# Performance work log

Hardware: AMD Instinct MI355X
Metric: run time of the kernel (lower is better)

Reference implementation:

```python
import jax, jax.numpy as jnp
import numpy as np

TEMPERATURE = 0.1
WINDOW = 7  # torch loop: k in range(1, min(8, seq_len - i)) -> offsets 1..7


def _normalize(x, axis=-1, eps=1e-12):
    # F.normalize: x / max(||x||, eps)
    n = jnp.linalg.norm(x, axis=axis, keepdims=True)
    return x / jnp.maximum(n, eps)


def setup_inputs() -> dict:
    key = jax.random.key(0)
    k1, k2 = jax.random.split(key, 2)
    states = jax.random.normal(k1, (4, 16, 1024, 256), dtype=jnp.float32)
    patterns = jax.random.normal(k2, (64, 256), dtype=jnp.float32)
    transfer_weights = jnp.zeros((16, 64, 64), dtype=jnp.float32)
    return {"states": states, "patterns": patterns, "transfer_weights": transfer_weights}


def _forward(states, patterns, transfer_weights):
    b, h, s, d = states.shape
    # --- detect_patterns: similarity to normalized pattern library + softmax ---
    sims = jnp.einsum('bhsd,pd->bhsp', states, _normalize(patterns))
    pattern_scores = jax.nn.softmax(sims / TEMPERATURE, axis=-1)  # [b,h,s,p]

    # --- compute_routing_scores: grad of states.sum() wrt states is ones ->
    #     grad_norm = ||ones||_2 over dim = sqrt(d) (constant), softmax over seq ---
    grad_norm = jnp.full((b, h, s), jnp.sqrt(jnp.float32(d)), dtype=states.dtype)
    routing_scores = jax.nn.softmax(grad_norm / TEMPERATURE, axis=-1)  # uniform [b,h,s]

    # --- optimize_routing: windowed min-plus shortest-path DP ---
    # torch keeps distances [b,h,s,s] but every slice along dim 2 is identical
    # (init and updates only index the last axis), so carry a [b,h,s] vector
    # and broadcast at the end. Pad by WINDOW so near-end updates land in pad.
    inf = jnp.float32(np.inf)
    dist0 = jnp.full((b, h, s + WINDOW), inf, dtype=states.dtype).at[..., 0].set(0.0)
    cost_pad = jnp.pad(-routing_scores, ((0, 0), (0, 0), (0, WINDOW)))

    def step(dist, i):
        cur = jax.lax.dynamic_slice_in_dim(dist, i, 1, axis=-1)          # [b,h,1]
        win = jax.lax.dynamic_slice_in_dim(dist, i + 1, WINDOW, axis=-1)  # [b,h,W]
        c = jax.lax.dynamic_slice_in_dim(cost_pad, i + 1, WINDOW, axis=-1)
        new = jnp.minimum(win, cur + c)
        dist = jax.lax.dynamic_update_slice_in_dim(dist, new, i + 1, axis=-1)
        return dist, None

    dist, _ = jax.lax.scan(step, dist0, jnp.arange(s - 1))
    d_final = dist[..., :s]                                  # [b,h,s]
    optimal_routes = jnp.broadcast_to(d_final[:, :, None, :], (b, h, s, s))

    return routing_scores, optimal_routes, transfer_weights, pattern_scores


def reference(states, patterns, transfer_weights):
    return _forward(states, patterns, transfer_weights)
```

## Files before the change

kernel.cpp:

```cpp
#include <hip/hip_runtime.h>
#include <math.h>

constexpr int B = 4, H = 16, S = 1024, D = 256, P = 64;
constexpr long long N_ROWS = (long long)B * H * S;
constexpr long long OFF_RT = 0;
constexpr long long SZ_RT  = N_ROWS;
constexpr long long OFF_OR = OFF_RT + SZ_RT;
constexpr long long SZ_OR  = N_ROWS * (long long)S;
constexpr long long OFF_TW = OFF_OR + SZ_OR;
constexpr long long SZ_TW  = 16LL * 64 * 64;
constexpr long long OFF_PS = OFF_TW + SZ_TW;

typedef _Float16 half8   __attribute__((ext_vector_type(8)));
typedef _Float16 half4v  __attribute__((ext_vector_type(4)));
typedef float    floatx4 __attribute__((ext_vector_type(4)));

constexpr int BSTRIDE = 264;

constexpr int GEMM_BLOCKS  = 512;
constexpr int SMALL_BLOCKS = 128;
constexpr int ROUTE_F4_PER_THREAD = 16;
constexpr int ROUTE_BLOCKS =
    (int)((SZ_OR / 4) / (256LL * ROUTE_F4_PER_THREAD));

__global__ __launch_bounds__(256) void k_gemm(
        const float* __restrict__ states,
        const float* __restrict__ pat,
        float* __restrict__ out) {
    __shared__ _Float16 smem[2 * P * BSTRIDE];
    int blk = blockIdx.x;
    int tid = threadIdx.x;

    _Float16* smH = smem;
    _Float16* smL = smem + P * BSTRIDE;

    int wave = tid >> 6;
    int lane = tid & 63;

    #pragma unroll 4
    for (int i = 0; i < 16; ++i) {
        int p = wave * 16 + i;
        floatx4 v = ((const floatx4*)(pat + (long long)p * D))[lane];
        float ss = v.x * v.x + v.y * v.y + v.z * v.z + v.w * v.w;
        #pragma unroll
        for (int m = 1; m < 64; m <<= 1) ss += __shfl_xor(ss, m, 64);
        float scale = 10.0f / fmaxf(sqrtf(ss), 1e-12f);
        half4v hh, ll;
        #pragma unroll
        for (int j = 0; j < 4; ++j) {
            float a = v[j] * scale;
            _Float16 h = (_Float16)a;
            hh[j] = h;
            ll[j] = (_Float16)(a - (float)h);
        }
        *(half4v*)&smH[p * BSTRIDE + lane * 4] = hh;
        *(half4v*)&smL[p * BSTRIDE + lane * 4] = ll;
    }
    __syncthreads();

    int q = lane >> 4;
    int m = lane & 15;
    long long row0 = (long long)blk * 128 + wave * 32;
    const float* __restrict__ arow0 = states + (row0 + m) * D + q * 8;
    const float* __restrict__ arow1 = arow0 + 16 * D;

    floatx4 acc0[4] = {floatx4{0,0,0,0}, floatx4{0,0,0,0},
                       floatx4{0,0,0,0}, floatx4{0,0,0,0}};
    floatx4 acc1[4] = {floatx4{0,0,0,0}, floatx4{0,0,0,0},
                       floatx4{0,0,0,0}, floatx4{0,0,0,0}};

    float4 n0 = *(const float4*)(arow0);
    float4 n1 = *(const float4*)(arow0 + 4);
    float4 n2 = *(const float4*)(arow1);
    float4 n3 = *(const float4*)(arow1 + 4);
    #pragma unroll
    for (int kk = 0; kk < 8; ++kk) {
        float av0[8] = { n0.x, n0.y, n0.z, n0.w, n1.x, n1.y, n1.z, n1.w };
        float av1[8] = { n2.x, n2.y, n2.z, n2.w, n3.x, n3.y, n3.z, n3.w };
        if (kk < 7) {
            n0 = *(const float4*)(arow0 + (kk + 1) * 32);
            n1 = *(const float4*)(arow0 + (kk + 1) * 32 + 4);
            n2 = *(const float4*)(arow1 + (kk + 1) * 32);
            n3 = *(const float4*)(arow1 + (kk + 1) * 32 + 4);
        }
        half8 ah0, al0, ah1, al1;
        #pragma unroll
        for (int j = 0; j < 8; ++j) {
            _Float16 h0 = (_Float16)av0[j];
            ah0[j] = h0;
            al0[j] = (_Float16)(av0[j] - (float)h0);
            _Float16 h1 = (_Float16)av1[j];
            ah1[j] = h1;
            al1[j] = (_Float16)(av1[j] - (float)h1);
        }
        #pragma unroll
        for (int t = 0; t < 4; ++t) {
            int boff = (t * 16 + m) * BSTRIDE + kk * 32 + q * 8;
            half8 bh = *(const half8*)&smH[boff];
            half8 bl = *(const half8*)&smL[boff];
            acc0[t] = __builtin_amdgcn_mfma_f32_16x16x32_f16(ah0, bh, acc0[t], 0, 0, 0);
            acc0[t] = __builtin_amdgcn_mfma_f32_16x16x32_f16(al0, bh, acc0[t], 0, 0, 0);
            acc0[t] = __builtin_amdgcn_mfma_f32_16x16x32_f16(ah0, bl, acc0[t], 0, 0, 0);
            acc1[t] = __builtin_amdgcn_mfma_f32_16x16x32_f16(ah1, bh, acc1[t], 0, 0, 0);
            acc1[t] = __builtin_amdgcn_mfma_f32_16x16x32_f16(al1, bh, acc1[t], 0, 0, 0);
            acc1[t] = __builtin_amdgcn_mfma_f32_16x16x32_f16(ah1, bl, acc1[t], 0, 0, 0);
        }
    }

    float* out_ps = out + OFF_PS;
    #pragma unroll
    for (int set = 0; set < 2; ++set) {
        floatx4* acc = set ? acc1 : acc0;
        long long rbase = row0 + set * 16;
        #pragma unroll
        for (int r = 0; r < 4; ++r) {
            float mx = fmaxf(fmaxf(acc[0][r], acc[1][r]),
                             fmaxf(acc[2][r], acc[3][r]));
            #pragma unroll
            for (int msk = 1; msk < 16; msk <<= 1)
                mx = fmaxf(mx, __shfl_xor(mx, msk, 64));
            float e[4];
            float s = 0.0f;
            #pragma unroll
            for (int t = 0; t < 4; ++t) { e[t] = __expf(acc[t][r] - mx); s += e[t]; }
            #pragma unroll
            for (int msk = 1; msk < 16; msk <<= 1) s += __shfl_xor(s, msk, 64);
            float inv = 1.0f / s;
            long long row = rbase + q * 4 + r;
            #pragma unroll
            for (int t = 0; t < 4; ++t) {
                out_ps[row * P + t * 16 + m] = e[t] * inv;
            }
        }
    }
}

__global__ __launch_bounds__(256) void k_fill(
        const floatx4* __restrict__ tw,
        float* __restrict__ out) {
    int blk = blockIdx.x;
    int tid = threadIdx.x;

    if (blk < SMALL_BLOCKS) {
        int i = blk * 256 + tid;
        constexpr int Q = (int)(SZ_RT / 4);
        if (i < Q) {
            floatx4 v = { 0.0009765625f, 0.0009765625f,
                          0.0009765625f, 0.0009765625f };
            ((floatx4*)(out + OFF_RT))[i] = v;
        } else {
            ((floatx4*)(out + OFF_TW))[i - Q] = tw[i - Q];
        }
        return;
    }

    long long rb = blk - SMALL_BLOCKS;
    float b0 = (float)(tid << 2) * (-0.0009765625f);
    floatx4 v;
    v.x = b0;
    v.y = b0 - 0.0009765625f;
    v.z = b0 - 0.001953125f;
    v.w = b0 - 0.0029296875f;
    floatx4* dst = (floatx4*)(out + OFF_OR)
                 + rb * (256LL * ROUTE_F4_PER_THREAD) + tid;
    #pragma unroll
    for (int k = 0; k < ROUTE_F4_PER_THREAD; ++k)
        dst[k * 256] = v;
}

extern "C" void kernel_launch(void* const* d_in, const int* in_sizes, int n_in,
                              void* d_out, int out_size, void* d_ws, size_t ws_size,
                              hipStream_t stream) {
    const float* states   = (const float*)d_in[0];
    const float* patterns = (const float*)d_in[1];
    const float* transfer = (const float*)d_in[2];
    float* out = (float*)d_out;

    k_gemm<<<dim3(GEMM_BLOCKS), dim3(256), 0, stream>>>(states, patterns, out);
    k_fill<<<dim3(SMALL_BLOCKS + ROUTE_BLOCKS), dim3(256), 0, stream>>>(
        (const floatx4*)transfer, out);
}
```

Measured before the change: 343.6 us.

## Fuse GEMM and fill kernels into one launch with one-float4-per-thread route fill

Merges the pattern-score GEMM kernel and the constant-fill kernel into a single launch, dispatching by block index: route-fill blocks first, then small fills, then GEMM blocks. The route fill now writes one float4 per thread across 65536 blocks instead of 16 per thread across 4096 blocks. The aim is to drop a launch and overlap the compute-bound GEMM with the write-bound fill. In exchange, the fill blocks also reserve the GEMM's large static LDS allocation, which may limit occupancy, and many more tiny blocks add scheduling overhead.

```diff
diff --git a/kernel.cpp b/kernel.cpp
--- a/kernel.cpp
+++ b/kernel.cpp
@@ -17,20 +17,45 @@
 
 constexpr int BSTRIDE = 264;
 
-constexpr int GEMM_BLOCKS  = 512;
-constexpr int SMALL_BLOCKS = 128;
-constexpr int ROUTE_F4_PER_THREAD = 16;
-constexpr int ROUTE_BLOCKS =
-    (int)((SZ_OR / 4) / (256LL * ROUTE_F4_PER_THREAD));
+constexpr int ROUTE_BLOCKS  = 65536;
+constexpr int SMALL_BLOCKS  = 128;
+constexpr int GEMM_BLOCKS   = 512;
 
-__global__ __launch_bounds__(256) void k_gemm(
+__global__ __launch_bounds__(256) void k_all(
         const float* __restrict__ states,
         const float* __restrict__ pat,
+        const floatx4* __restrict__ tw,
         float* __restrict__ out) {
     __shared__ _Float16 smem[2 * P * BSTRIDE];
     int blk = blockIdx.x;
     int tid = threadIdx.x;
 
+    if (blk < ROUTE_BLOCKS) {
+        long long i = (long long)blk * 256 + tid;
+        int j0 = (int)((i << 2) & (S - 1));
+        float b0 = (float)j0 * (-0.0009765625f);
+        floatx4 v;
+        v.x = b0;
+        v.y = b0 - 0.0009765625f;
+        v.z = b0 - 0.001953125f;
+        v.w = b0 - 0.0029296875f;
+        ((floatx4*)(out + OFF_OR))[i] = v;
+        return;
+    }
+    if (blk < ROUTE_BLOCKS + SMALL_BLOCKS) {
+        int i = (blk - ROUTE_BLOCKS) * 256 + tid;
+        constexpr int Q = (int)(SZ_RT / 4);
+        if (i < Q) {
+            floatx4 v = { 0.0009765625f, 0.0009765625f,
+                          0.0009765625f, 0.0009765625f };
+            ((floatx4*)(out + OFF_RT))[i] = v;
+        } else {
+            ((floatx4*)(out + OFF_TW))[i - Q] = tw[i - Q];
+        }
+        return;
+    }
+
+    int gb = blk - ROUTE_BLOCKS - SMALL_BLOCKS;
     _Float16* smH = smem;
     _Float16* smL = smem + P * BSTRIDE;
 
@@ -60,7 +85,7 @@
 
     int q = lane >> 4;
     int m = lane & 15;
-    long long row0 = (long long)blk * 128 + wave * 32;
+    long long row0 = (long long)gb * 128 + wave * 32;
     const float* __restrict__ arow0 = states + (row0 + m) * D + q * 8;
     const float* __restrict__ arow1 = arow0 + 16 * D;
 
@@ -135,39 +160,6 @@
     }
 }
 
-__global__ __launch_bounds__(256) void k_fill(
-        const floatx4* __restrict__ tw,
-        float* __restrict__ out) {
-    int blk = blockIdx.x;
-    int tid = threadIdx.x;
-
-    if (blk < SMALL_BLOCKS) {
-        int i = blk * 256 + tid;
-        constexpr int Q = (int)(SZ_RT / 4);
-        if (i < Q) {
-            floatx4 v = { 0.0009765625f, 0.0009765625f,
-                          0.0009765625f, 0.0009765625f };
-            ((floatx4*)(out + OFF_RT))[i] = v;
-        } else {
-            ((floatx4*)(out + OFF_TW))[i - Q] = tw[i - Q];
-        }
-        return;
-    }
-
-    long long rb = blk - SMALL_BLOCKS;
-    float b0 = (float)(tid << 2) * (-0.0009765625f);
-    floatx4 v;
-    v.x = b0;
-    v.y = b0 - 0.0009765625f;
-    v.z = b0 - 0.001953125f;
-    v.w = b0 - 0.0029296875f;
-    floatx4* dst = (floatx4*)(out + OFF_OR)
-                 + rb * (256LL * ROUTE_F4_PER_THREAD) + tid;
-    #pragma unroll
-    for (int k = 0; k < ROUTE_F4_PER_THREAD; ++k)
-        dst[k * 256] = v;
-}
-
 extern "C" void kernel_launch(void* const* d_in, const int* in_sizes, int n_in,
                               void* d_out, int out_size, void* d_ws, size_t ws_size,
                               hipStream_t stream) {
@@ -176,7 +168,6 @@
     const float* transfer = (const float*)d_in[2];
     float* out = (float*)d_out;
 
-    k_gemm<<<dim3(GEMM_BLOCKS), dim3(256), 0, stream>>>(states, patterns, out);
-    k_fill<<<dim3(SMALL_BLOCKS + ROUTE_BLOCKS), dim3(256), 0, stream>>>(
-        (const floatx4*)transfer, out);
+    k_all<<<dim3(ROUTE_BLOCKS + SMALL_BLOCKS + GEMM_BLOCKS), dim3(256), 0,
+            stream>>>(states, patterns, (const floatx4*)transfer, out);
 }
```

Result: faster. 328.4 us (-4.4%).
